# Performance work log

Measured on AMD Instinct MI355X. Metric: run time of the kernel, lower is better.

## Reference

```python
import jax, jax.numpy as jnp
import numpy as np

N_NODES = 50000
N_EDGES = 800000
HEADS = 4
OUT_CH = 64
NEG_SLOPE = 0.2  # PyG GATConv default


def gat_conv(x, edge_index, W, att_src, att_dst, bias):
    """PyG GATConv (concat=True, add_self_loops=True, eval mode).
    x: [N, F_in], edge_index: [2, E] (row 0 = src, row 1 = dst).
    W: [F_in, H*C], att_src/att_dst: [1, H, C], bias: [H*C].
    """
    n = x.shape[0]
    loops = jnp.arange(n, dtype=edge_index.dtype)
    src = jnp.concatenate([edge_index[0], loops])  # [E+N]
    dst = jnp.concatenate([edge_index[1], loops])

    h = (x @ W).reshape(n, HEADS, OUT_CH)           # [N, H, C]
    a_src = jnp.sum(h * att_src, axis=-1)           # [N, H]
    a_dst = jnp.sum(h * att_dst, axis=-1)           # [N, H]

    e = a_src[src] + a_dst[dst]                     # [E+N, H]
    e = jax.nn.leaky_relu(e, NEG_SLOPE)

    # segment softmax over incoming edges of each dst node
    e_max = jax.ops.segment_max(e, dst, num_segments=n)   # [N, H]
    e_exp = jnp.exp(e - e_max[dst])
    denom = jax.ops.segment_sum(e_exp, dst, num_segments=n)
    alpha = e_exp / (denom[dst] + 1e-16)            # [E+N, H]

    msg = h[src] * alpha[:, :, None]                # [E+N, H, C]
    out = jax.ops.segment_sum(msg, dst, num_segments=n)   # [N, H, C]
    return out.reshape(n, HEADS * OUT_CH) + bias


def setup_inputs() -> dict:
    key = jax.random.key(0)
    ks = jax.random.split(key, 10)
    d_in = 256
    d_hid = HEADS * OUT_CH  # 256
    s_in = 1.0 / np.sqrt(d_in)
    s_hid = 1.0 / np.sqrt(d_hid)
    return {
        "x": jax.random.normal(ks[0], (N_NODES, d_in), dtype=jnp.float32),
        "edge_index": jax.random.randint(ks[1], (2, N_EDGES), 0, N_NODES, dtype=jnp.int32),
        "W1": jax.random.normal(ks[2], (d_in, d_hid), dtype=jnp.float32) * s_in,
        "att_src1": jax.random.normal(ks[3], (1, HEADS, OUT_CH), dtype=jnp.float32) * s_hid,
        "att_dst1": jax.random.normal(ks[4], (1, HEADS, OUT_CH), dtype=jnp.float32) * s_hid,
        "b1": jnp.zeros((d_hid,), dtype=jnp.float32),
        "W2": jax.random.normal(ks[5], (d_hid, d_hid), dtype=jnp.float32) * s_hid,
        "att_src2": jax.random.normal(ks[6], (1, HEADS, OUT_CH), dtype=jnp.float32) * s_hid,
        "att_dst2": jax.random.normal(ks[7], (1, HEADS, OUT_CH), dtype=jnp.float32) * s_hid,
        "b2": jnp.zeros((d_hid,), dtype=jnp.float32),
    }


def reference(x, edge_index, W1, att_src1, att_dst1, b1, W2, att_src2, att_dst2, b2):
    # layer 1 + ELU (dropout is identity in eval mode)
    h = gat_conv(x, edge_index, W1, att_src1, att_dst1, b1)
    h = jax.nn.elu(h)
    # layer 2 + ELU
    h = gat_conv(h, edge_index, W2, att_src2, att_dst2, b2)
    h = jax.nn.elu(h)
    return h
```

## Files before the change

kernel.cpp:

```cpp
#include <hip/hip_runtime.h>
#include <hip/hip_bf16.h>

#define N_NODES 50000
#define N_EDGES 800000

typedef __attribute__((ext_vector_type(8))) short short8;
typedef __attribute__((ext_vector_type(4))) float floatx4;

__device__ __forceinline__ ushort f2bf(float f) {
    uint u = __float_as_uint(f);
    uint r = u + 0x7FFFu + ((u >> 16) & 1u);
    return (ushort)(r >> 16);
}
__device__ __forceinline__ float bfu2f(ushort h) {
    return __uint_as_float(((uint)h) << 16);
}
__device__ __forceinline__ float bflo(uint u) { return __uint_as_float(u << 16); }
__device__ __forceinline__ float bfhi(uint u) { return __uint_as_float(u & 0xffff0000u); }
__device__ __forceinline__ float lrelu(float e) { return e >= 0.f ? e : 0.2f * e; }

__global__ void deg_kernel(const int* __restrict__ dst, int* __restrict__ cnt, int E) {
    int i = blockIdx.x * blockDim.x + threadIdx.x;
    if (i < E) atomicAdd(&cnt[dst[i]], 1);
}

__global__ __launch_bounds__(256) void scan1_kernel(const int* __restrict__ cnt,
                                                    int* __restrict__ excl,
                                                    int* __restrict__ partial, int n) {
    __shared__ int sd[256];
    int tid = threadIdx.x;
    int i = blockIdx.x * 256 + tid;
    int v = (i < n) ? cnt[i] : 0;
    sd[tid] = v;
    __syncthreads();
    #pragma unroll
    for (int off = 1; off < 256; off <<= 1) {
        int t = (tid >= off) ? sd[tid - off] : 0;
        __syncthreads();
        sd[tid] += t;
        __syncthreads();
    }
    if (i < n) excl[i] = sd[tid] - v;
    if (tid == 255) partial[blockIdx.x] = sd[255];
}

__global__ __launch_bounds__(256) void scan2_kernel(int* __restrict__ partial, int nb) {
    __shared__ int sd[256];
    int tid = threadIdx.x;
    int v = (tid < nb) ? partial[tid] : 0;
    sd[tid] = v;
    __syncthreads();
    #pragma unroll
    for (int off = 1; off < 256; off <<= 1) {
        int t = (tid >= off) ? sd[tid - off] : 0;
        __syncthreads();
        sd[tid] += t;
        __syncthreads();
    }
    if (tid < nb) partial[tid] = sd[tid] - v;
}

__global__ __launch_bounds__(256) void scan3_kernel(const int* __restrict__ excl,
                                                    const int* __restrict__ partial,
                                                    int* __restrict__ row_ptr,
                                                    int* __restrict__ row_tmp, int n) {
    int i = blockIdx.x * 256 + threadIdx.x;
    if (i < n) {
        int v = excl[i] + partial[blockIdx.x];
        row_ptr[i] = v;
        row_tmp[i] = v;
    }
    if (i == 0) row_ptr[n] = N_EDGES;
}

__global__ void scatter_kernel(const int* __restrict__ src, const int* __restrict__ dst,
                               int* __restrict__ row_tmp, int* __restrict__ sorted_src,
                               int* __restrict__ sorted_dst, int E) {
    int i = blockIdx.x * blockDim.x + threadIdx.x;
    if (i < E) {
        int d = dst[i];
        int p = atomicAdd(&row_tmp[d], 1);
        sorted_src[p] = src[i];
        sorted_dst[p] = d;
    }
}

__global__ void prep_w(const float* __restrict__ W1, const float* __restrict__ W2,
                       ushort* __restrict__ Wt1_hi, ushort* __restrict__ Wt1_lo,
                       ushort* __restrict__ Wt2_hi, ushort* __restrict__ Wt2_lo) {
    int n = threadIdx.x, k = blockIdx.x & 255;
    const float* W = (blockIdx.x < 256) ? W1 : W2;
    ushort* Wh = (blockIdx.x < 256) ? Wt1_hi : Wt2_hi;
    ushort* Wl = (blockIdx.x < 256) ? Wt1_lo : Wt2_lo;
    float v = W[k * 256 + n];
    ushort hb = f2bf(v);
    Wh[n * 256 + k] = hb;
    Wl[n * 256 + k] = f2bf(v - bfu2f(hb));
}

__global__ __launch_bounds__(256) void gemm_att_kernel(const float* __restrict__ A,
                                                       const ushort* __restrict__ Wt_hi,
                                                       const ushort* __restrict__ Wt_lo,
                                                       const float* __restrict__ att_s,
                                                       const float* __restrict__ att_d,
                                                       ushort* __restrict__ H,
                                                       float* __restrict__ a_src,
                                                       float* __restrict__ a_dst, int M) {
    const int ROWP = 40;
    __shared__ ushort hi_s[128 * ROWP];
    __shared__ ushort lo_s[128 * ROWP];
    const int tid = threadIdx.x;
    const int wave = tid >> 6, lane = tid & 63;
    const int quad = lane >> 4, l16 = lane & 15;
    const int brow = blockIdx.x * 64;
    const int coff = blockIdx.y * 128;
    const int mrow = brow + wave * 16 + l16;
    const int mload = (mrow < M) ? mrow : (M - 1);

    floatx4 acc[8];
    #pragma unroll
    for (int t = 0; t < 8; t++) acc[t] = (floatx4){0.f, 0.f, 0.f, 0.f};

    for (int k0 = 0; k0 < 256; k0 += 32) {
        __syncthreads();
        {
            int t = tid & 127;
            const ushort* g = ((tid < 128) ? Wt_hi : Wt_lo) + (size_t)(coff + t) * 256 + k0;
            ushort* d = ((tid < 128) ? hi_s : lo_s) + t * ROWP;
            #pragma unroll
            for (int i = 0; i < 4; i++)
                *reinterpret_cast<short8*>(d + i * 8) =
                    *reinterpret_cast<const short8*>(g + i * 8);
        }
        __syncthreads();
        const float* ap = A + (size_t)mload * 256 + k0 + quad * 8;
        float4 a0 = *reinterpret_cast<const float4*>(ap);
        float4 a1 = *reinterpret_cast<const float4*>(ap + 4);
        float av[8] = {a0.x, a0.y, a0.z, a0.w, a1.x, a1.y, a1.z, a1.w};
        short8 a_hi, a_lo;
        #pragma unroll
        for (int j = 0; j < 8; j++) {
            ushort hb = f2bf(av[j]);
            a_hi[j] = (short)hb;
            a_lo[j] = (short)f2bf(av[j] - bfu2f(hb));
        }
        #pragma unroll
        for (int t = 0; t < 8; t++) {
            int roff = (t * 16 + l16) * ROWP + quad * 8;
            short8 b_hi = *reinterpret_cast<const short8*>(&hi_s[roff]);
            short8 b_lo = *reinterpret_cast<const short8*>(&lo_s[roff]);
            acc[t] = __builtin_amdgcn_mfma_f32_16x16x32_bf16(a_hi, b_hi, acc[t], 0, 0, 0);
            acc[t] = __builtin_amdgcn_mfma_f32_16x16x32_bf16(a_hi, b_lo, acc[t], 0, 0, 0);
            acc[t] = __builtin_amdgcn_mfma_f32_16x16x32_bf16(a_lo, b_hi, acc[t], 0, 0, 0);
        }
    }
    const int hb = blockIdx.y * 2;
    float ps[2][4] = {}, pd[2][4] = {};
    #pragma unroll
    for (int t = 0; t < 8; t++) {
        int hh = t >> 2;
        float as_v = att_s[coff + t * 16 + l16];
        float ad_v = att_d[coff + t * 16 + l16];
        #pragma unroll
        for (int r = 0; r < 4; r++) {
            ps[hh][r] += acc[t][r] * as_v;
            pd[hh][r] += acc[t][r] * ad_v;
        }
    }
    #pragma unroll
    for (int off = 1; off < 16; off <<= 1) {
        #pragma unroll
        for (int hh = 0; hh < 2; hh++)
            #pragma unroll
            for (int r = 0; r < 4; r++) {
                ps[hh][r] += __shfl_xor(ps[hh][r], off, 64);
                pd[hh][r] += __shfl_xor(pd[hh][r], off, 64);
            }
    }
    if (l16 == 0) {
        #pragma unroll
        for (int r = 0; r < 4; r++) {
            int m = brow + wave * 16 + quad * 4 + r;
            if (m < M) {
                #pragma unroll
                for (int hh = 0; hh < 2; hh++) {
                    a_src[m * 4 + hb + hh] = ps[hh][r];
                    a_dst[m * 4 + hb + hh] = pd[hh][r];
                }
            }
        }
    }
    #pragma unroll
    for (int t = 0; t < 8; t++) {
        int col = coff + t * 16 + l16;
        int c = col & 63, hh = col >> 6;
        #pragma unroll
        for (int r = 0; r < 4; r++) {
            int m = brow + wave * 16 + quad * 4 + r;
            if (m < M) H[(size_t)m * 256 + c * 4 + hh] = f2bf(acc[t][r]);
        }
    }
}

__global__ __launch_bounds__(256) void ew_kernel(const float* __restrict__ a_src,
                                                 const float* __restrict__ a_dst,
                                                 const int* __restrict__ sorted_src,
                                                 const int* __restrict__ sorted_dst,
                                                 float* __restrict__ ew, int E) {
    int j = blockIdx.x * 256 + threadIdx.x;
    if (j >= E) return;
    int s = sorted_src[j], d = sorted_dst[j];
    float4 as_ = *reinterpret_cast<const float4*>(a_src + (size_t)s * 4);
    float4 ad_ = *reinterpret_cast<const float4*>(a_dst + (size_t)d * 4);
    float4 w;
    w.x = __expf(lrelu(as_.x + ad_.x));
    w.y = __expf(lrelu(as_.y + ad_.y));
    w.z = __expf(lrelu(as_.z + ad_.z));
    w.w = __expf(lrelu(as_.w + ad_.w));
    *reinterpret_cast<float4*>(ew + (size_t)j * 4) = w;
}

__global__ __launch_bounds__(256) void agg_kernel(const ushort* __restrict__ H,
                                                  const float* __restrict__ a_src,
                                                  const float* __restrict__ a_dst,
                                                  const int* __restrict__ row_ptr,
                                                  const int* __restrict__ sorted_src,
                                                  const float* __restrict__ ew,
                                                  const float* __restrict__ bias,
                                                  float* __restrict__ out, int N) {
    int wave = threadIdx.x >> 6, lane = threadIdx.x & 63;
    int half = lane >> 5, hl = lane & 31;
    int i = blockIdx.x * 4 + wave;
    if (i >= N) return;
    float4 asv = *reinterpret_cast<const float4*>(a_src + (size_t)i * 4);
    float4 adv = *reinterpret_cast<const float4*>(a_dst + (size_t)i * 4);
    float ws0 = __expf(lrelu(asv.x + adv.x)), ws1 = __expf(lrelu(asv.y + adv.y));
    float ws2 = __expf(lrelu(asv.z + adv.z)), ws3 = __expf(lrelu(asv.w + adv.w));
    int start = row_ptr[i], end = row_ptr[i + 1];

    float a0 = 0.f, a1 = 0.f, a2 = 0.f, a3 = 0.f;
    float b0 = 0.f, b1 = 0.f, b2 = 0.f, b3 = 0.f;
    float dp0 = 0.f, dp1 = 0.f, dp2 = 0.f, dp3 = 0.f;

    for (int j = start + half; j < end; j += 2) {
        int sj = sorted_src[j];
        float4 w = *reinterpret_cast<const float4*>(ew + (size_t)j * 4);
        uint4 hv = *reinterpret_cast<const uint4*>(H + (size_t)sj * 256 + hl * 8);
        a0 += w.x * bflo(hv.x); a1 += w.y * bfhi(hv.x);
        a2 += w.z * bflo(hv.y); a3 += w.w * bfhi(hv.y);
        b0 += w.x * bflo(hv.z); b1 += w.y * bfhi(hv.z);
        b2 += w.z * bflo(hv.w); b3 += w.w * bfhi(hv.w);
        dp0 += w.x; dp1 += w.y; dp2 += w.z; dp3 += w.w;
    }
    a0 += __shfl_xor(a0, 32, 64); a1 += __shfl_xor(a1, 32, 64);
    a2 += __shfl_xor(a2, 32, 64); a3 += __shfl_xor(a3, 32, 64);
    b0 += __shfl_xor(b0, 32, 64); b1 += __shfl_xor(b1, 32, 64);
    b2 += __shfl_xor(b2, 32, 64); b3 += __shfl_xor(b3, 32, 64);
    dp0 += __shfl_xor(dp0, 32, 64); dp1 += __shfl_xor(dp1, 32, 64);
    dp2 += __shfl_xor(dp2, 32, 64); dp3 += __shfl_xor(dp3, 32, 64);
    {
        uint4 hv = *reinterpret_cast<const uint4*>(H + (size_t)i * 256 + hl * 8);
        a0 += ws0 * bflo(hv.x); a1 += ws1 * bfhi(hv.x);
        a2 += ws2 * bflo(hv.y); a3 += ws3 * bfhi(hv.y);
        b0 += ws0 * bflo(hv.z); b1 += ws1 * bfhi(hv.z);
        b2 += ws2 * bflo(hv.w); b3 += ws3 * bfhi(hv.w);
    }
    float r0 = 1.f / (dp0 + ws0 + 1e-16f), r1 = 1.f / (dp1 + ws1 + 1e-16f);
    float r2 = 1.f / (dp2 + ws2 + 1e-16f), r3 = 1.f / (dp3 + ws3 + 1e-16f);
    float* op = out + (size_t)i * 256 + hl * 2;
    float va = (half == 0) ? a0 : a2, vb = (half == 0) ? b0 : b2;
    float ra = (half == 0) ? r0 : r2;
    float va2 = (half == 0) ? a1 : a3, vb2 = (half == 0) ? b1 : b3;
    float ra2 = (half == 0) ? r1 : r3;
    int hofs = half * 128;
    float2 o;
    float v;
    v = va * ra + bias[hofs + 2 * hl];      o.x = (v > 0.f) ? v : expm1f(v);
    v = vb * ra + bias[hofs + 2 * hl + 1];  o.y = (v > 0.f) ? v : expm1f(v);
    *reinterpret_cast<float2*>(op + hofs) = o;
    v = va2 * ra2 + bias[hofs + 64 + 2 * hl];     o.x = (v > 0.f) ? v : expm1f(v);
    v = vb2 * ra2 + bias[hofs + 64 + 2 * hl + 1]; o.y = (v > 0.f) ? v : expm1f(v);
    *reinterpret_cast<float2*>(op + hofs + 64) = o;
}

extern "C" void kernel_launch(void* const* d_in, const int* in_sizes, int n_in,
                              void* d_out, int out_size, void* d_ws, size_t ws_size,
                              hipStream_t stream) {
    const float* x      = (const float*)d_in[0];
    const int*   eidx   = (const int*)d_in[1];
    const float* W1     = (const float*)d_in[2];
    const float* att_s1 = (const float*)d_in[3];
    const float* att_d1 = (const float*)d_in[4];
    const float* b1     = (const float*)d_in[5];
    const float* W2     = (const float*)d_in[6];
    const float* att_s2 = (const float*)d_in[7];
    const float* att_d2 = (const float*)d_in[8];
    const float* b2     = (const float*)d_in[9];
    float* out = (float*)d_out;

    const int N = N_NODES, E = N_EDGES;
    char* ws = (char*)d_ws;
    size_t off = 0;
    auto alloc = [&](size_t bytes) -> void* {
        void* p = ws + off;
        off += (bytes + 255) & ~(size_t)255;
        return p;
    };
    ushort* h       = (ushort*)alloc((size_t)N * 256 * sizeof(ushort));
    float*  ew      = (float*) alloc((size_t)E * 4 * sizeof(float));
    float*  a_src   = (float*) alloc((size_t)N * 4 * sizeof(float));
    float*  a_dst   = (float*) alloc((size_t)N * 4 * sizeof(float));
    int*    cnt     = (int*)   alloc((size_t)N * sizeof(int));
    int*    row_ptr = (int*)   alloc((size_t)(N + 1) * sizeof(int));
    int*    row_tmp = (int*)   alloc((size_t)N * sizeof(int));
    int*    sorted  = (int*)   alloc((size_t)E * sizeof(int));
    int*    sortedd = (int*)   alloc((size_t)E * sizeof(int));
    int*    excl    = (int*)   alloc((size_t)N * sizeof(int));
    int*    partial = (int*)   alloc(256 * sizeof(int));
    ushort* Wt1_hi  = (ushort*)alloc(256 * 256 * sizeof(ushort));
    ushort* Wt1_lo  = (ushort*)alloc(256 * 256 * sizeof(ushort));
    ushort* Wt2_hi  = (ushort*)alloc(256 * 256 * sizeof(ushort));
    ushort* Wt2_lo  = (ushort*)alloc(256 * 256 * sizeof(ushort));
    float*  x2      = out;
    (void)ws_size; (void)in_sizes; (void)n_in; (void)out_size;

    const int* e_src = eidx;
    const int* e_dst = eidx + E;
    const int nsb = (N + 255) / 256;
    const int neb = (E + 255) / 256;

    prep_w<<<512, 256, 0, stream>>>(W1, W2, Wt1_hi, Wt1_lo, Wt2_hi, Wt2_lo);
    hipMemsetAsync(cnt, 0, N * sizeof(int), stream);
    deg_kernel<<<neb, 256, 0, stream>>>(e_dst, cnt, E);
    scan1_kernel<<<nsb, 256, 0, stream>>>(cnt, excl, partial, N);
    scan2_kernel<<<1, 256, 0, stream>>>(partial, nsb);
    scan3_kernel<<<nsb, 256, 0, stream>>>(excl, partial, row_ptr, row_tmp, N);
    scatter_kernel<<<neb, 256, 0, stream>>>(e_src, e_dst, row_tmp, sorted, sortedd, E);

    dim3 ggrid((N + 63) / 64, 2);
    int nblk = (N + 3) / 4;
    gemm_att_kernel<<<ggrid, 256, 0, stream>>>(x, Wt1_hi, Wt1_lo, att_s1, att_d1,
                                               h, a_src, a_dst, N);
    ew_kernel<<<neb, 256, 0, stream>>>(a_src, a_dst, sorted, sortedd, ew, E);
    agg_kernel<<<nblk, 256, 0, stream>>>(h, a_src, a_dst, row_ptr, sorted, ew, b1, x2, N);
    gemm_att_kernel<<<ggrid, 256, 0, stream>>>(x2, Wt2_hi, Wt2_lo, att_s2, att_d2,
                                               h, a_src, a_dst, N);
    ew_kernel<<<neb, 256, 0, stream>>>(a_src, a_dst, sorted, sortedd, ew, E);
    agg_kernel<<<nblk, 256, 0, stream>>>(h, a_src, a_dst, row_ptr, sorted, ew, b2, out, N);
}
```

Baseline: 475.3 us.

## Store H in natural layout and give each lane one head in aggregation

The GEMM epilogue now writes H in the natural [node][head*64+c] layout instead of the interleaved c*4+head layout. The aggregation kernel is reorganised so each lane owns eight contiguous channels of a single head, loading one scalar edge weight instead of a float4. It unrolls the edge loop by two for more memory-level parallelism and uses a grid-stride loop over a fixed 2048 blocks. The cost is that the self-loop, normalisation and output work now runs only in half the lanes, and the uint4 gather per lane is unchanged.

```diff
diff --git a/kernel.cpp b/kernel.cpp
--- a/kernel.cpp
+++ b/kernel.cpp
@@ -193,11 +193,10 @@
     #pragma unroll
     for (int t = 0; t < 8; t++) {
         int col = coff + t * 16 + l16;
-        int c = col & 63, hh = col >> 6;
         #pragma unroll
         for (int r = 0; r < 4; r++) {
             int m = brow + wave * 16 + quad * 4 + r;
-            if (m < M) H[(size_t)m * 256 + c * 4 + hh] = f2bf(acc[t][r]);
+            if (m < M) H[(size_t)m * 256 + col] = f2bf(acc[t][r]);
         }
     }
 }
@@ -228,59 +227,72 @@
                                                   const float* __restrict__ ew,
                                                   const float* __restrict__ bias,
                                                   float* __restrict__ out, int N) {
-    int wave = threadIdx.x >> 6, lane = threadIdx.x & 63;
-    int half = lane >> 5, hl = lane & 31;
-    int i = blockIdx.x * 4 + wave;
-    if (i >= N) return;
-    float4 asv = *reinterpret_cast<const float4*>(a_src + (size_t)i * 4);
-    float4 adv = *reinterpret_cast<const float4*>(a_dst + (size_t)i * 4);
-    float ws0 = __expf(lrelu(asv.x + adv.x)), ws1 = __expf(lrelu(asv.y + adv.y));
-    float ws2 = __expf(lrelu(asv.z + adv.z)), ws3 = __expf(lrelu(asv.w + adv.w));
-    int start = row_ptr[i], end = row_ptr[i + 1];
-
-    float a0 = 0.f, a1 = 0.f, a2 = 0.f, a3 = 0.f;
-    float b0 = 0.f, b1 = 0.f, b2 = 0.f, b3 = 0.f;
-    float dp0 = 0.f, dp1 = 0.f, dp2 = 0.f, dp3 = 0.f;
-
-    for (int j = start + half; j < end; j += 2) {
-        int sj = sorted_src[j];
-        float4 w = *reinterpret_cast<const float4*>(ew + (size_t)j * 4);
-        uint4 hv = *reinterpret_cast<const uint4*>(H + (size_t)sj * 256 + hl * 8);
-        a0 += w.x * bflo(hv.x); a1 += w.y * bfhi(hv.x);
-        a2 += w.z * bflo(hv.y); a3 += w.w * bfhi(hv.y);
-        b0 += w.x * bflo(hv.z); b1 += w.y * bfhi(hv.z);
-        b2 += w.z * bflo(hv.w); b3 += w.w * bfhi(hv.w);
-        dp0 += w.x; dp1 += w.y; dp2 += w.z; dp3 += w.w;
-    }
-    a0 += __shfl_xor(a0, 32, 64); a1 += __shfl_xor(a1, 32, 64);
-    a2 += __shfl_xor(a2, 32, 64); a3 += __shfl_xor(a3, 32, 64);
-    b0 += __shfl_xor(b0, 32, 64); b1 += __shfl_xor(b1, 32, 64);
-    b2 += __shfl_xor(b2, 32, 64); b3 += __shfl_xor(b3, 32, 64);
-    dp0 += __shfl_xor(dp0, 32, 64); dp1 += __shfl_xor(dp1, 32, 64);
-    dp2 += __shfl_xor(dp2, 32, 64); dp3 += __shfl_xor(dp3, 32, 64);
-    {
-        uint4 hv = *reinterpret_cast<const uint4*>(H + (size_t)i * 256 + hl * 8);
-        a0 += ws0 * bflo(hv.x); a1 += ws1 * bfhi(hv.x);
-        a2 += ws2 * bflo(hv.y); a3 += ws3 * bfhi(hv.y);
-        b0 += ws0 * bflo(hv.z); b1 += ws1 * bfhi(hv.z);
-        b2 += ws2 * bflo(hv.w); b3 += ws3 * bfhi(hv.w);
-    }
-    float r0 = 1.f / (dp0 + ws0 + 1e-16f), r1 = 1.f / (dp1 + ws1 + 1e-16f);
-    float r2 = 1.f / (dp2 + ws2 + 1e-16f), r3 = 1.f / (dp3 + ws3 + 1e-16f);
-    float* op = out + (size_t)i * 256 + hl * 2;
-    float va = (half == 0) ? a0 : a2, vb = (half == 0) ? b0 : b2;
-    float ra = (half == 0) ? r0 : r2;
-    float va2 = (half == 0) ? a1 : a3, vb2 = (half == 0) ? b1 : b3;
-    float ra2 = (half == 0) ? r1 : r3;
-    int hofs = half * 128;
-    float2 o;
-    float v;
-    v = va * ra + bias[hofs + 2 * hl];      o.x = (v > 0.f) ? v : expm1f(v);
-    v = vb * ra + bias[hofs + 2 * hl + 1];  o.y = (v > 0.f) ? v : expm1f(v);
-    *reinterpret_cast<float2*>(op + hofs) = o;
-    v = va2 * ra2 + bias[hofs + 64 + 2 * hl];     o.x = (v > 0.f) ? v : expm1f(v);
-    v = vb2 * ra2 + bias[hofs + 64 + 2 * hl + 1]; o.y = (v > 0.f) ? v : expm1f(v);
-    *reinterpret_cast<float2*>(op + hofs + 64) = o;
+    const int wave = threadIdx.x >> 6, lane = threadIdx.x & 63;
+    const int half = lane >> 5, hl = lane & 31;
+    const int head = hl >> 3;
+    const int hoff = head * 64 + (hl & 7) * 8;
+
+    for (int i = blockIdx.x * 4 + wave; i < N; i += gridDim.x * 4) {
+        float wself = __expf(lrelu(a_src[i * 4 + head] + a_dst[i * 4 + head]));
+        int start = row_ptr[i], end = row_ptr[i + 1];
+        float c0 = 0.f, c1 = 0.f, c2 = 0.f, c3 = 0.f;
+        float c4 = 0.f, c5 = 0.f, c6 = 0.f, c7 = 0.f;
+        float dp = 0.f;
+        int j = start + half;
+        for (; j + 2 < end; j += 4) {
+            int s0 = sorted_src[j], s1 = sorted_src[j + 2];
+            float w0 = ew[(size_t)j * 4 + head];
+            float w1 = ew[(size_t)(j + 2) * 4 + head];
+            uint4 h0 = *reinterpret_cast<const uint4*>(H + (size_t)s0 * 256 + hoff);
+            uint4 h1 = *reinterpret_cast<const uint4*>(H + (size_t)s1 * 256 + hoff);
+            c0 += w0 * bflo(h0.x); c1 += w0 * bfhi(h0.x);
+            c2 += w0 * bflo(h0.y); c3 += w0 * bfhi(h0.y);
+            c4 += w0 * bflo(h0.z); c5 += w0 * bfhi(h0.z);
+            c6 += w0 * bflo(h0.w); c7 += w0 * bfhi(h0.w);
+            dp += w0;
+            c0 += w1 * bflo(h1.x); c1 += w1 * bfhi(h1.x);
+            c2 += w1 * bflo(h1.y); c3 += w1 * bfhi(h1.y);
+            c4 += w1 * bflo(h1.z); c5 += w1 * bfhi(h1.z);
+            c6 += w1 * bflo(h1.w); c7 += w1 * bfhi(h1.w);
+            dp += w1;
+        }
+        for (; j < end; j += 2) {
+            int s0 = sorted_src[j];
+            float w0 = ew[(size_t)j * 4 + head];
+            uint4 h0 = *reinterpret_cast<const uint4*>(H + (size_t)s0 * 256 + hoff);
+            c0 += w0 * bflo(h0.x); c1 += w0 * bfhi(h0.x);
+            c2 += w0 * bflo(h0.y); c3 += w0 * bfhi(h0.y);
+            c4 += w0 * bflo(h0.z); c5 += w0 * bfhi(h0.z);
+            c6 += w0 * bflo(h0.w); c7 += w0 * bfhi(h0.w);
+            dp += w0;
+        }
+        c0 += __shfl_xor(c0, 32, 64); c1 += __shfl_xor(c1, 32, 64);
+        c2 += __shfl_xor(c2, 32, 64); c3 += __shfl_xor(c3, 32, 64);
+        c4 += __shfl_xor(c4, 32, 64); c5 += __shfl_xor(c5, 32, 64);
+        c6 += __shfl_xor(c6, 32, 64); c7 += __shfl_xor(c7, 32, 64);
+        dp += __shfl_xor(dp, 32, 64);
+        if (half == 0) {
+            uint4 hv = *reinterpret_cast<const uint4*>(H + (size_t)i * 256 + hoff);
+            c0 += wself * bflo(hv.x); c1 += wself * bfhi(hv.x);
+            c2 += wself * bflo(hv.y); c3 += wself * bfhi(hv.y);
+            c4 += wself * bflo(hv.z); c5 += wself * bfhi(hv.z);
+            c6 += wself * bflo(hv.w); c7 += wself * bfhi(hv.w);
+            float r = 1.f / (dp + wself + 1e-16f);
+            const float* bp = bias + hoff;
+            float4 o;
+            float v;
+            v = c0 * r + bp[0]; o.x = (v > 0.f) ? v : expm1f(v);
+            v = c1 * r + bp[1]; o.y = (v > 0.f) ? v : expm1f(v);
+            v = c2 * r + bp[2]; o.z = (v > 0.f) ? v : expm1f(v);
+            v = c3 * r + bp[3]; o.w = (v > 0.f) ? v : expm1f(v);
+            *reinterpret_cast<float4*>(out + (size_t)i * 256 + hoff) = o;
+            v = c4 * r + bp[4]; o.x = (v > 0.f) ? v : expm1f(v);
+            v = c5 * r + bp[5]; o.y = (v > 0.f) ? v : expm1f(v);
+            v = c6 * r + bp[6]; o.z = (v > 0.f) ? v : expm1f(v);
+            v = c7 * r + bp[7]; o.w = (v > 0.f) ? v : expm1f(v);
+            *reinterpret_cast<float4*>(out + (size_t)i * 256 + hoff + 4) = o;
+        }
+    }
 }
 
 extern "C" void kernel_launch(void* const* d_in, const int* in_sizes, int n_in,
@@ -338,13 +350,13 @@
     scatter_kernel<<<neb, 256, 0, stream>>>(e_src, e_dst, row_tmp, sorted, sortedd, E);
 
     dim3 ggrid((N + 63) / 64, 2);
-    int nblk = (N + 3) / 4;
+    const int ablk = 2048;
     gemm_att_kernel<<<ggrid, 256, 0, stream>>>(x, Wt1_hi, Wt1_lo, att_s1, att_d1,
                                                h, a_src, a_dst, N);
     ew_kernel<<<neb, 256, 0, stream>>>(a_src, a_dst, sorted, sortedd, ew, E);
-    agg_kernel<<<nblk, 256, 0, stream>>>(h, a_src, a_dst, row_ptr, sorted, ew, b1, x2, N);
+    agg_kernel<<<ablk, 256, 0, stream>>>(h, a_src, a_dst, row_ptr, sorted, ew, b1, x2, N);
     gemm_att_kernel<<<ggrid, 256, 0, stream>>>(x2, Wt2_hi, Wt2_lo, att_s2, att_d2,
                                                h, a_src, a_dst, N);
     ew_kernel<<<neb, 256, 0, stream>>>(a_src, a_dst, sorted, sortedd, ew, E);
-    agg_kernel<<<nblk, 256, 0, stream>>>(h, a_src, a_dst, row_ptr, sorted, ew, b2, out, N);
-}
+    agg_kernel<<<ablk, 256, 0, stream>>>(h, a_src, a_dst, row_ptr, sorted, ew, b2, out, N);
+}
```

Measured after the change: 478.8 us. Within noise of the previous version (+0.7%).
